# Performance work log

Hardware: AMD Instinct MI355X
Metric: run time of the kernel (lower is better)

The kernel has to match this reference:

```python
import jax, jax.numpy as jnp
import numpy as np

B, N, CTX = 1024, 50000, 96
D_IN, D_MAIN, D_BLOCK, OUT = 128, 256, 512, 10
EPS = 1e-5


def _ln(h, g, b):
    m = jnp.mean(h, -1, keepdims=True)
    v = jnp.var(h, -1, keepdims=True)
    return (h - m) / jnp.sqrt(v + EPS) * g + b


def _forward(fl, candidate_y, context_size):
    (x, candidate_x, W_lin, b_lin,
     enc0_W1, enc0_b1, enc0_W2, enc0_b2,
     enc1_g, enc1_b, enc1_W1, enc1_b1, enc1_W2, enc1_b2,
     mix_g, mix_b, K_W, K_b, label_emb,
     T_W1, T_b1, T_W2,
     p0_g, p0_b, p0_W1, p0_b1, p0_W2, p0_b2,
     p1_g, p1_b, p1_W1, p1_b1, p1_W2, p1_b2,
     head_g, head_b, head_W, head_bias) = fl

    def block(h, g, b, W1, b1, W2, b2, prenorm):
        t = _ln(h, g, b) if prenorm else h
        return h + (jax.nn.relu(t @ W1 + b1) @ W2 + b2)

    def encode(h):
        h = h @ W_lin + b_lin
        h = block(h, None, None, enc0_W1, enc0_b1, enc0_W2, enc0_b2, False)
        h = block(h, enc1_g, enc1_b, enc1_W1, enc1_b1, enc1_W2, enc1_b2, True)
        k = _ln(h, mix_g, mix_b) @ K_W + K_b
        return h, k

    cand_k = encode(candidate_x)[1]          # [N, D]
    h, k = encode(x)                          # [B, D] each
    # exact L2 kNN search (faiss IndexFlatL2 equivalent), indices are non-differentiable
    d2 = (jnp.sum(k * k, -1, keepdims=True) - 2.0 * (k @ cand_k.T)
          + jnp.sum(cand_k * cand_k, -1))    # [B, N]
    idx = jax.lax.stop_gradient(jax.lax.top_k(-d2, context_size)[1])  # [B, C]
    ck = cand_k[idx]                          # [B, C, D]
    sim = (-jnp.sum(k * k, -1, keepdims=True)
           + 2.0 * jnp.einsum('bd,bcd->bc', k, ck)
           - jnp.sum(ck * ck, -1))            # [B, C]
    probs = jax.nn.softmax(sim, -1)
    y_emb = label_emb[candidate_y[idx]]       # [B, C, D]
    vals = y_emb + jax.nn.relu((k[:, None, :] - ck) @ T_W1 + T_b1) @ T_W2
    h = h + jnp.einsum('bc,bcd->bd', probs, vals)
    h = block(h, p0_g, p0_b, p0_W1, p0_b1, p0_W2, p0_b2, True)
    h = block(h, p1_g, p1_b, p1_W1, p1_b1, p1_W2, p1_b2, True)
    return jax.nn.relu(_ln(h, head_g, head_b)) @ head_W + head_bias


def setup_inputs() -> dict:
    key = jax.random.key(0)
    ks = iter(jax.random.split(key, 64))
    def W(shape, fan_in):
        s = 1.0 / np.sqrt(fan_in)
        return jax.random.uniform(next(ks), shape, jnp.float32, -s, s)
    z = lambda *s: jnp.zeros(s, jnp.float32)
    o = lambda *s: jnp.ones(s, jnp.float32)
    d = {
        'x': jax.random.normal(next(ks), (B, D_IN), jnp.float32),
        'candidate_x': jax.random.normal(next(ks), (N, D_IN), jnp.float32),
        'candidate_y': jax.random.randint(next(ks), (N,), 0, OUT),
        'context_size': CTX,
        'W_lin': W((D_IN, D_MAIN), D_IN), 'b_lin': z(D_MAIN),
        'enc0_W1': W((D_MAIN, D_BLOCK), D_MAIN), 'enc0_b1': z(D_BLOCK),
        'enc0_W2': W((D_BLOCK, D_MAIN), D_BLOCK), 'enc0_b2': z(D_MAIN),
        'enc1_g': o(D_MAIN), 'enc1_b': z(D_MAIN),
        'enc1_W1': W((D_MAIN, D_BLOCK), D_MAIN), 'enc1_b1': z(D_BLOCK),
        'enc1_W2': W((D_BLOCK, D_MAIN), D_BLOCK), 'enc1_b2': z(D_MAIN),
        'mix_g': o(D_MAIN), 'mix_b': z(D_MAIN),
        'K_W': W((D_MAIN, D_MAIN), D_MAIN), 'K_b': z(D_MAIN),
        'label_emb': jax.random.uniform(next(ks), (OUT, D_MAIN), jnp.float32, -1.0, 1.0),
        'T_W1': W((D_MAIN, D_BLOCK), D_MAIN), 'T_b1': z(D_BLOCK),
        'T_W2': W((D_BLOCK, D_MAIN), D_BLOCK),
        'p0_g': o(D_MAIN), 'p0_b': z(D_MAIN),
        'p0_W1': W((D_MAIN, D_BLOCK), D_MAIN), 'p0_b1': z(D_BLOCK),
        'p0_W2': W((D_BLOCK, D_MAIN), D_BLOCK), 'p0_b2': z(D_MAIN),
        'p1_g': o(D_MAIN), 'p1_b': z(D_MAIN),
        'p1_W1': W((D_MAIN, D_BLOCK), D_MAIN), 'p1_b1': z(D_BLOCK),
        'p1_W2': W((D_BLOCK, D_MAIN), D_BLOCK), 'p1_b2': z(D_MAIN),
        'head_g': o(D_MAIN), 'head_b': z(D_MAIN),
        'head_W': W((D_MAIN, OUT), D_MAIN), 'head_bias': z(OUT),
    }
    return d


def reference(x, candidate_x, candidate_y, context_size, W_lin, b_lin,
              enc0_W1, enc0_b1, enc0_W2, enc0_b2,
              enc1_g, enc1_b, enc1_W1, enc1_b1, enc1_W2, enc1_b2,
              mix_g, mix_b, K_W, K_b, label_emb,
              T_W1, T_b1, T_W2,
              p0_g, p0_b, p0_W1, p0_b1, p0_W2, p0_b2,
              p1_g, p1_b, p1_W1, p1_b1, p1_W2, p1_b2,
              head_g, head_b, head_W, head_bias):
    fl = (x, candidate_x, W_lin, b_lin,
          enc0_W1, enc0_b1, enc0_W2, enc0_b2,
          enc1_g, enc1_b, enc1_W1, enc1_b1, enc1_W2, enc1_b2,
          mix_g, mix_b, K_W, K_b, label_emb,
          T_W1, T_b1, T_W2,
          p0_g, p0_b, p0_W1, p0_b1, p0_W2, p0_b2,
          p1_g, p1_b, p1_W1, p1_b1, p1_W2, p1_b2,
          head_g, head_b, head_W, head_bias)
    return _forward(fl, candidate_y, context_size)
```

## Files before the change

### kernel.cpp

```cpp
#include <hip/hip_runtime.h>
#include <hip/hip_bf16.h>
#include <cstdint>
#include <cstddef>

#define B_ROWS 1024
#define N_CAND 50000
#define CTX    96
#define D_IN   128
#define D_MAIN 256
#define D_BLOCK 512
#define N_OUT  10
#define LN_EPS 1e-5f
#define MAXTIE 4096
#define NTOT   (N_CAND + B_ROWS)

typedef unsigned short u16;
typedef __attribute__((ext_vector_type(8))) short bf16x8;
typedef __attribute__((ext_vector_type(4))) float f32x4;

__device__ __forceinline__ u16 bf16_bits(float f) {
    __hip_bfloat16 h = __float2bfloat16(f);
    return *reinterpret_cast<u16*>(&h);
}
__device__ __forceinline__ float bits_to_f32(u16 b) {
    unsigned u = ((unsigned)b) << 16;
    return __uint_as_float(u);
}
__device__ __forceinline__ void split_f32(float v, u16& h, u16& l) {
    h = bf16_bits(v);
    l = bf16_bits(v - bits_to_f32(h));
}
__device__ __forceinline__ float join_f32(u16 h, u16 l) {
    return bits_to_f32(h) + bits_to_f32(l);
}
__device__ __forceinline__ unsigned f2u_mono(float f) {
    unsigned u = __float_as_uint(f);
    return u ^ ((u & 0x80000000u) ? 0xFFFFFFFFu : 0x80000000u);
}

__device__ __forceinline__ void load_lds_16B(const void* gp, void* lp) {
    __builtin_amdgcn_global_load_lds((const __attribute__((address_space(1))) void*)gp,
                                     (__attribute__((address_space(3))) void*)lp,
                                     16, 0, 0);
}

template<bool RELU, bool HAS_BIAS, bool HAS_RES, bool KEY16,
         bool OUT_F32, bool OUT_SPLIT, bool OUT_B16, bool A_LO, bool B_LO, bool MXFAST>
__global__ __launch_bounds__(512)
void gemm_split_nt(const u16* __restrict__ Ah, const u16* __restrict__ Al,
                   const u16* __restrict__ Bh, const u16* __restrict__ Bl,
                   const float* __restrict__ bias, const float* __restrict__ Rm,
                   float* __restrict__ Cf, u16* __restrict__ Ch, u16* __restrict__ Cl,
                   int M, int N, int K)
{
    constexpr int N_LOAD = (2 + (A_LO ? 1 : 0) + (B_LO ? 1 : 0)) * 4096;
    constexpr bool STAGED = KEY16 || OUT_SPLIT || OUT_B16;
    constexpr int CS_STRIDE = 136;
    constexpr int CS_SIZE = 128 * CS_STRIDE;
    constexpr int SM_MIN = STAGED ? CS_SIZE : 0;
    constexpr int SM_U16 = (2 * N_LOAD > SM_MIN) ? 2 * N_LOAD : SM_MIN;
    __shared__ __align__(16) u16 smem[SM_U16];

    constexpr int offAsl = A_LO ? 4096 : 0;
    constexpr int offBsh = 4096 * (1 + (A_LO ? 1 : 0));
    constexpr int offBsl = offBsh + (B_LO ? 4096 : 0);

    const int tid  = threadIdx.x;
    const int wave = tid >> 6, lane = tid & 63;

    int bm, bn;
    if constexpr (MXFAST) {
        const unsigned nbm = gridDim.x;
        const unsigned total = nbm * gridDim.y;
        const unsigned h = blockIdx.x + nbm * blockIdx.y;
        unsigned mi = blockIdx.x, ni = blockIdx.y;
        if ((total & 7u) == 0u) {
            const unsigned per = total >> 3;
            const unsigned virt = (h & 7u) * per + (h >> 3);
            mi = virt % nbm;
            ni = virt / nbm;
        }
        bm = (int)mi * 128; bn = (int)ni * 128;
    } else {
        bm = blockIdx.y * 128; bn = blockIdx.x * 128;
    }

    const int wm = (wave >> 2) * 64, wn = (wave & 3) * 32;
    const int l16 = lane & 15, quad = lane >> 4;

    const int srow = lane >> 2;
    const int scol = (lane & 3) * 8;

    const int r0 = wave * 16 + srow;
    int ga0 = bm + r0; if (ga0 > M - 1) ga0 = M - 1;
    int gb0 = bn + r0; if (gb0 > N - 1) gb0 = N - 1;
    const size_t offA0 = (size_t)ga0 * K + scol;
    const size_t offB0 = (size_t)gb0 * K + scol;
    const int ldsR0 = (wave * 16) * 32;

    auto stage = [&](int buf, int k0) {
        u16* base = smem + buf * N_LOAD;
        load_lds_16B(Ah + offA0 + k0, &base[ldsR0]);
        if constexpr (A_LO)
            load_lds_16B(Al + offA0 + k0, &base[offAsl + ldsR0]);
        load_lds_16B(Bh + offB0 + k0, &base[offBsh + ldsR0]);
        if constexpr (B_LO)
            load_lds_16B(Bl + offB0 + k0, &base[offBsl + ldsR0]);
    };

    f32x4 acc[4][2];
    #pragma unroll
    for (int i = 0; i < 4; ++i)
        #pragma unroll
        for (int j = 0; j < 2; ++j)
            acc[i][j] = (f32x4){0.f, 0.f, 0.f, 0.f};

    stage(0, 0);
    int cur = 0;
    for (int k0 = 0; k0 < K; k0 += 32) {
        __syncthreads();

        const u16* Ash = smem + cur * N_LOAD;
        const u16* Asl = Ash + offAsl;
        const u16* Bsh = Ash + offBsh;
        const u16* Bsl = Ash + offBsl;

        bf16x8 ah[4], al[4], bh[2], bl[2];
        #pragma unroll
        for (int i = 0; i < 4; ++i) {
            ah[i] = *(const bf16x8*)&Ash[(wm + i * 16 + l16) * 32 + quad * 8];
            if constexpr (A_LO)
                al[i] = *(const bf16x8*)&Asl[(wm + i * 16 + l16) * 32 + quad * 8];
        }
        #pragma unroll
        for (int j = 0; j < 2; ++j) {
            bh[j] = *(const bf16x8*)&Bsh[(wn + j * 16 + l16) * 32 + quad * 8];
            if constexpr (B_LO)
                bl[j] = *(const bf16x8*)&Bsl[(wn + j * 16 + l16) * 32 + quad * 8];
        }

        if (k0 + 32 < K) stage(cur ^ 1, k0 + 32);

        #pragma unroll
        for (int i = 0; i < 4; ++i)
            #pragma unroll
            for (int j = 0; j < 2; ++j) {
                acc[i][j] = __builtin_amdgcn_mfma_f32_16x16x32_bf16(ah[i], bh[j], acc[i][j], 0, 0, 0);
                if constexpr (A_LO)
                    acc[i][j] = __builtin_amdgcn_mfma_f32_16x16x32_bf16(al[i], bh[j], acc[i][j], 0, 0, 0);
                if constexpr (B_LO)
                    acc[i][j] = __builtin_amdgcn_mfma_f32_16x16x32_bf16(ah[i], bl[j], acc[i][j], 0, 0, 0);
            }
        cur ^= 1;
    }

    float bvj[2];
    #pragma unroll
    for (int j = 0; j < 2; ++j) {
        const int n = bn + wn + j * 16 + l16;
        bvj[j] = ((HAS_BIAS || KEY16) && n < N) ? bias[n] : 0.f;
    }
    auto compute = [&](int i, int j, int r) -> float {
        float v = acc[i][j][r];
        if (KEY16) return -2.f * v + bvj[j];
        if (HAS_BIAS) v += bvj[j];
        if (RELU)     v = fmaxf(v, 0.f);
        if (HAS_RES) {
            const int n = bn + wn + j * 16 + l16;
            const int m = bm + wm + i * 16 + quad * 4 + r;
            v += Rm[(size_t)m * N + n];
        }
        return v;
    };

    if constexpr (OUT_F32) {
        #pragma unroll
        for (int j = 0; j < 2; ++j) {
            const int n = bn + wn + j * 16 + l16;
            if (n >= N) continue;
            #pragma unroll
            for (int i = 0; i < 4; ++i)
                #pragma unroll
                for (int r = 0; r < 4; ++r) {
                    const int m = bm + wm + i * 16 + quad * 4 + r;
                    if (m >= M) continue;
                    Cf[(size_t)m * N + n] = compute(i, j, r);
                }
        }
    }

    if constexpr (STAGED) {
        u16* Cs = smem;
        const int phases = OUT_SPLIT ? 2 : 1;
        for (int ph = 0; ph < phases; ++ph) {
            __syncthreads();
            #pragma unroll
            for (int j = 0; j < 2; ++j) {
                const int nl = wn + j * 16 + l16;
                if (bn + nl >= N) continue;
                #pragma unroll
                for (int i = 0; i < 4; ++i)
                    #pragma unroll
                    for (int r = 0; r < 4; ++r) {
                        const int ml = wm + i * 16 + quad * 4 + r;
                        if (bm + ml >= M) continue;
                        const float v = compute(i, j, r);
                        u16 out;
                        if (KEY16)        out = (u16)(f2u_mono(v) >> 16);
                        else if (OUT_B16) out = bf16_bits(v);
                        else { u16 h, l; split_f32(v, h, l); out = ph ? l : h; }
                        Cs[ml * CS_STRIDE + nl] = out;
                    }
            }
            __syncthreads();
            u16* dstB = (OUT_SPLIT && ph) ? Cl : Ch;
            const int row = tid >> 2, seg = (tid & 3) * 32;
            const int m = bm + row;
            if (m < M) {
                const int ncols = N - bn;
                u16* dst = dstB + (size_t)m * N + bn + seg;
                const u16* srcp = &Cs[row * CS_STRIDE + seg];
                if (ncols >= 128) {
                    #pragma unroll
                    for (int c = 0; c < 4; ++c)
                        *reinterpret_cast<uint4*>(dst + c * 8) =
                            *reinterpret_cast<const uint4*>(srcp + c * 8);
                } else {
                    for (int e = 0; e < 32; ++e)
                        if (seg + e < ncols) dst[e] = srcp[e];
                }
            }
        }
    }
}

__global__ __launch_bounds__(256)
void gemm_head(const float* __restrict__ A, const float* __restrict__ Bm,
               const float* __restrict__ bias, float* __restrict__ C,
               int M, int N, int K)
{
    __shared__ float As[16][64];
    __shared__ float Bs[16][64];
    const int tid = threadIdx.x;
    const int bm = blockIdx.y * 64;

    const int a_m = tid >> 2;
    const int a_k = (tid & 3) << 2;
    const int b_k = tid >> 4;
    const int b_n = (tid & 15) << 2;
    const int my = (tid >> 4) << 2;
    const int nx = (tid & 15) << 2;

    float acc[4][4] = {};

    for (int k0 = 0; k0 < K; k0 += 16) {
        float4 av = make_float4(0.f,0.f,0.f,0.f);
        const int gm = bm + a_m;
        if (gm < M) av = *(const float4*)(A + (size_t)gm * K + k0 + a_k);
        As[a_k+0][a_m]=av.x; As[a_k+1][a_m]=av.y; As[a_k+2][a_m]=av.z; As[a_k+3][a_m]=av.w;

        float4 bv = make_float4(0.f,0.f,0.f,0.f);
        const float* bp = Bm + (size_t)(k0 + b_k) * N + b_n;
        if (b_n + 0 < N) bv.x = bp[0];
        if (b_n + 1 < N) bv.y = bp[1];
        if (b_n + 2 < N) bv.z = bp[2];
        if (b_n + 3 < N) bv.w = bp[3];
        *(float4*)&Bs[b_k][b_n] = bv;

        __syncthreads();
        #pragma unroll
        for (int k = 0; k < 16; ++k) {
            const float4 a4 = *(const float4*)&As[k][my];
            const float4 b4 = *(const float4*)&Bs[k][nx];
            const float a[4] = {a4.x,a4.y,a4.z,a4.w};
            const float b[4] = {b4.x,b4.y,b4.z,b4.w};
            #pragma unroll
            for (int i = 0; i < 4; ++i)
                #pragma unroll
                for (int j = 0; j < 4; ++j)
                    acc[i][j] = fmaf(a[i], b[j], acc[i][j]);
        }
        __syncthreads();
    }

    #pragma unroll
    for (int i = 0; i < 4; ++i) {
        const int m = bm + my + i;
        if (m >= M) continue;
        #pragma unroll
        for (int j = 0; j < 4; ++j) {
            const int n = nx + j;
            if (n >= N) continue;
            C[(size_t)m * N + n] = acc[i][j] + bias[n];
        }
    }
}

template<bool RELU, bool OUT_SPLIT>
__global__ __launch_bounds__(256)
void ln_kernel(const float* __restrict__ X, const float* __restrict__ g,
               const float* __restrict__ b, float* __restrict__ Yf,
               u16* __restrict__ Yh, u16* __restrict__ Yl)
{
    const int row = blockIdx.x, tid = threadIdx.x;
    const float x = X[(size_t)row * D_MAIN + tid];
    __shared__ float red[4];
    const int lane = tid & 63, wid = tid >> 6;

    float s = x;
    #pragma unroll
    for (int off = 32; off; off >>= 1) s += __shfl_down(s, off, 64);
    if (lane == 0) red[wid] = s;
    __syncthreads();
    const float mean = (red[0] + red[1] + red[2] + red[3]) * (1.f / D_MAIN);
    __syncthreads();

    const float xm = x - mean;
    s = xm * xm;
    #pragma unroll
    for (int off = 32; off; off >>= 1) s += __shfl_down(s, off, 64);
    if (lane == 0) red[wid] = s;
    __syncthreads();
    const float var = (red[0] + red[1] + red[2] + red[3]) * (1.f / D_MAIN);

    float y = xm / sqrtf(var + LN_EPS) * g[tid] + b[tid];
    if (RELU) y = fmaxf(y, 0.f);
    if (OUT_SPLIT) {
        u16 h, l; split_f32(y, h, l);
        Yh[(size_t)row * D_MAIN + tid] = h;
        Yl[(size_t)row * D_MAIN + tid] = l;
    } else {
        Yf[(size_t)row * D_MAIN + tid] = y;
    }
}

__global__ __launch_bounds__(64)
void cn2_kernel(const u16* __restrict__ ckh, const u16* __restrict__ ckl,
                float* __restrict__ out)
{
    const int row = blockIdx.x, lane = threadIdx.x;
    const ushort4 h4 = *(const ushort4*)(ckh + (size_t)row * D_MAIN + lane * 4);
    const ushort4 l4 = *(const ushort4*)(ckl + (size_t)row * D_MAIN + lane * 4);
    const float c0 = join_f32(h4.x, l4.x), c1 = join_f32(h4.y, l4.y);
    const float c2 = join_f32(h4.z, l4.z), c3 = join_f32(h4.w, l4.w);
    float s = c0*c0 + c1*c1 + c2*c2 + c3*c3;
    #pragma unroll
    for (int off = 32; off; off >>= 1) s += __shfl_down(s, off, 64);
    if (lane == 0) out[row] = s;
}

__global__ __launch_bounds__(256)
void f32_to_split_kernel(const float* __restrict__ src, u16* __restrict__ hi,
                         u16* __restrict__ lo, int n)
{
    int i = blockIdx.x * 256 + threadIdx.x;
    if (i < n) {
        u16 h, l; split_f32(src[i], h, l);
        hi[i] = h; lo[i] = l;
    }
}

struct TrD { const float* s; u16* dh; u16* dl; int R; int C; };
struct TrDs { TrD d[11]; };

__global__ __launch_bounds__(256)
void transpose_all_kernel(TrDs descs)
{
    const TrD D = descs.d[blockIdx.y];
    const int n = D.R * D.C;
    int idx = blockIdx.x * 256 + threadIdx.x;
    if (idx < n) {
        const int r = idx / D.C, c = idx % D.C;
        u16 h, l; split_f32(D.s[idx], h, l);
        D.dh[(size_t)c * D.R + r] = h;
        D.dl[(size_t)c * D.R + r] = l;
    }
}

__global__ __launch_bounds__(256)
void copy_rows_kernel(const float* __restrict__ src, float* __restrict__ dst, int n)
{
    int i = blockIdx.x * 256 + threadIdx.x;
    if (i < n) dst[i] = src[i];
}

__global__ __launch_bounds__(1024)
void topk96_u16_kernel(const u16* __restrict__ keys, int* __restrict__ idx_out,
                       int* __restrict__ tiebuf, int* __restrict__ tiecnt,
                       int* __restrict__ lesscnt)
{
    const int row = blockIdx.x;
    const u16* krow = keys + (size_t)row * N_CAND;
    const int tid = threadIdx.x;
    const int rep = tid & 63;

    __shared__ unsigned hist[256 * 64];
    __shared__ unsigned hsum[256];
    __shared__ unsigned sh_bin, sh_need;
    __shared__ int cntLess, cntEq;

    #pragma unroll
    for (int i = 0; i < 16; ++i) hist[tid + i * 1024] = 0;
    __syncthreads();
    for (int i = tid; i < N_CAND / 8; i += 1024) {
        const uint4 v = ((const uint4*)krow)[i];
        const unsigned w[4] = {v.x, v.y, v.z, v.w};
        #pragma unroll
        for (int e = 0; e < 4; ++e) {
            atomicAdd(&hist[(((w[e] >> 8) & 0xFFu)) * 64 + rep], 1u);
            atomicAdd(&hist[((w[e] >> 24)) * 64 + rep], 1u);
        }
    }
    __syncthreads();
    if (tid < 256) {
        unsigned s = 0;
        #pragma unroll
        for (int r = 0; r < 64; ++r) s += hist[tid * 64 + ((r + tid) & 63)];
        hsum[tid] = s;
    }
    __syncthreads();
    int need = CTX;
    if (tid < 64) {
        const unsigned b0 = hsum[tid*4+0], b1 = hsum[tid*4+1],
                       b2 = hsum[tid*4+2], b3 = hsum[tid*4+3];
        const unsigned lsum = b0 + b1 + b2 + b3;
        unsigned pre = lsum;
        #pragma unroll
        for (int off = 1; off < 64; off <<= 1) {
            const unsigned t = __shfl_up(pre, off, 64);
            if (tid >= off) pre += t;
        }
        const unsigned excl = pre - lsum;
        const unsigned nd = (unsigned)need;
        if (excl < nd && excl + lsum >= nd) {
            unsigned bin, rem;
            if      (excl + b0 >= nd)           { bin = tid*4+0; rem = nd - excl; }
            else if (excl + b0 + b1 >= nd)      { bin = tid*4+1; rem = nd - excl - b0; }
            else if (excl + b0 + b1 + b2 >= nd) { bin = tid*4+2; rem = nd - excl - b0 - b1; }
            else                                { bin = tid*4+3; rem = nd - excl - b0 - b1 - b2; }
            sh_bin = bin; sh_need = rem;
        }
    }
    __syncthreads();
    const unsigned hb = sh_bin;
    need = (int)sh_need;
    __syncthreads();

    #pragma unroll
    for (int i = 0; i < 16; ++i) hist[tid + i * 1024] = 0;
    __syncthreads();
    for (int i = tid; i < N_CAND / 8; i += 1024) {
        const uint4 v = ((const uint4*)krow)[i];
        const unsigned w[4] = {v.x, v.y, v.z, v.w};
        #pragma unroll
        for (int e = 0; e < 4; ++e) {
            const unsigned k0 = w[e] & 0xFFFFu, k1 = w[e] >> 16;
            if ((k0 >> 8) == hb) atomicAdd(&hist[(k0 & 255u) * 64 + rep], 1u);
            if ((k1 >> 8) == hb) atomicAdd(&hist[(k1 & 255u) * 64 + rep], 1u);
        }
    }
    __syncthreads();
    if (tid < 256) {
        unsigned s = 0;
        #pragma unroll
        for (int r = 0; r < 64; ++r) s += hist[tid * 64 + ((r + tid) & 63)];
        hsum[tid] = s;
    }
    __syncthreads();
    if (tid < 64) {
        const unsigned b0 = hsum[tid*4+0], b1 = hsum[tid*4+1],
                       b2 = hsum[tid*4+2], b3 = hsum[tid*4+3];
        const unsigned lsum = b0 + b1 + b2 + b3;
        unsigned pre = lsum;
        #pragma unroll
        for (int off = 1; off < 64; off <<= 1) {
            const unsigned t = __shfl_up(pre, off, 64);
            if (tid >= off) pre += t;
        }
        const unsigned excl = pre - lsum;
        const unsigned nd = (unsigned)need;
        if (excl < nd && excl + lsum >= nd) {
            unsigned bin, rem;
            if      (excl + b0 >= nd)           { bin = tid*4+0; rem = nd - excl; }
            else if (excl + b0 + b1 >= nd)      { bin = tid*4+1; rem = nd - excl - b0; }
            else if (excl + b0 + b1 + b2 >= nd) { bin = tid*4+2; rem = nd - excl - b0 - b1; }
            else                                { bin = tid*4+3; rem = nd - excl - b0 - b1 - b2; }
            sh_bin = bin; sh_need = rem;
        }
    }
    __syncthreads();
    const unsigned T16 = (hb << 8) | sh_bin;
    need = (int)sh_need;

    if (tid == 0) { cntLess = 0; cntEq = 0; }
    __syncthreads();

    for (int i = tid; i < N_CAND / 8; i += 1024) {
        const uint4 v = ((const uint4*)krow)[i];
        const unsigned w[4] = {v.x, v.y, v.z, v.w};
        #pragma unroll
        for (int e = 0; e < 4; ++e) {
            const unsigned k0 = w[e] & 0xFFFFu, k1 = w[e] >> 16;
            const int n0 = i * 8 + e * 2, n1 = n0 + 1;
            if (k0 < T16) {
                const int p = atomicAdd(&cntLess, 1);
                idx_out[row * CTX + p] = n0;
            } else if (k0 == T16) {
                const int p = atomicAdd(&cntEq, 1);
                if (p < MAXTIE) tiebuf[(size_t)row * MAXTIE + p] = n0;
            }
            if (k1 < T16) {
                const int p = atomicAdd(&cntLess, 1);
                idx_out[row * CTX + p] = n1;
            } else if (k1 == T16) {
                const int p = atomicAdd(&cntEq, 1);
                if (p < MAXTIE) tiebuf[(size_t)row * MAXTIE + p] = n1;
            }
        }
    }
    __syncthreads();
    if (tid == 0) {
        lesscnt[row] = cntLess;
        tiecnt[row] = (cntEq < MAXTIE) ? cntEq : MAXTIE;
    }
}

__global__ __launch_bounds__(256)
void select_kernel(const u16* __restrict__ kh, const u16* __restrict__ kl,
                   const u16* __restrict__ ckh, const u16* __restrict__ ckl,
                   const float* __restrict__ ck2,
                   const int* __restrict__ tiebuf, const int* __restrict__ tiecnt,
                   const int* __restrict__ lesscnt,
                   int* __restrict__ idx_out, float* __restrict__ probs)
{
    const int row = blockIdx.x;
    const int tid = threadIdx.x;
    const int T = tiecnt[row];
    const int less = lesscnt[row];
    const int need = CTX - less;

    __shared__ float kvs[D_MAIN];
    __shared__ int   sel[CTX];
    __shared__ float svals[CTX];
    __shared__ float sv[MAXTIE];
    __shared__ unsigned hist[256];
    __shared__ unsigned sh_bin, sh_need;
    __shared__ int c1, c2;

    if (tid < D_MAIN)
        kvs[tid] = join_f32(kh[(size_t)row * D_MAIN + tid], kl[(size_t)row * D_MAIN + tid]);
    if (tid < CTX && tid < less) sel[tid] = idx_out[row * CTX + tid];
    __syncthreads();

    if (T <= need) {
        for (int t = tid; t < T; t += 256) {
            sel[less + t] = tiebuf[(size_t)row * MAXTIE + t];
            idx_out[row * CTX + less + t] = sel[less + t];
        }
    } else {
        for (int t = tid; t < T; t += 256) {
            const int c = tiebuf[(size_t)row * MAXTIE + t];
            const u16* ch = ckh + (size_t)c * D_MAIN;
            const u16* cl = ckl + (size_t)c * D_MAIN;
            float s = 0.f;
            #pragma unroll 8
            for (int d = 0; d < D_MAIN; d += 4) {
                const ushort4 h4 = *(const ushort4*)(ch + d);
                const ushort4 l4 = *(const ushort4*)(cl + d);
                s += kvs[d+0] * join_f32(h4.x, l4.x) + kvs[d+1] * join_f32(h4.y, l4.y)
                   + kvs[d+2] * join_f32(h4.z, l4.z) + kvs[d+3] * join_f32(h4.w, l4.w);
            }
            sv[t] = ck2[c] - 2.f * s;
        }
        __syncthreads();

        unsigned prefix = 0;
        int plen = 0;
        int nd = need;
        for (int pass = 0; pass < 4; ++pass) {
            const int shift = 24 - 8 * pass;
            hist[tid] = 0;
            __syncthreads();
            for (int t = tid; t < T; t += 256) {
                const unsigned u = f2u_mono(sv[t]);
                if (plen == 0 || (u >> (32 - plen)) == prefix)
                    atomicAdd(&hist[(u >> shift) & 255u], 1u);
            }
            __syncthreads();
            if (tid < 64) {
                const unsigned b0 = hist[tid*4+0], b1 = hist[tid*4+1],
                               b2 = hist[tid*4+2], b3 = hist[tid*4+3];
                const unsigned lsum = b0 + b1 + b2 + b3;
                unsigned pre = lsum;
                #pragma unroll
                for (int off = 1; off < 64; off <<= 1) {
                    const unsigned tt = __shfl_up(pre, off, 64);
                    if (tid >= off) pre += tt;
                }
                const unsigned excl = pre - lsum;
                const unsigned ndu = (unsigned)nd;
                if (excl < ndu && excl + lsum >= ndu) {
                    unsigned bin, rem;
                    if      (excl + b0 >= ndu)           { bin = tid*4+0; rem = ndu - excl; }
                    else if (excl + b0 + b1 >= ndu)      { bin = tid*4+1; rem = ndu - excl - b0; }
                    else if (excl + b0 + b1 + b2 >= ndu) { bin = tid*4+2; rem = ndu - excl - b0 - b1; }
                    else                                 { bin = tid*4+3; rem = ndu - excl - b0 - b1 - b2; }
                    sh_bin = bin; sh_need = rem;
                }
            }
            __syncthreads();
            prefix = (prefix << 8) | sh_bin;
            nd = (int)sh_need;
            plen += 8;
            __syncthreads();
        }
        const unsigned Tf = prefix;
        const int nl2 = need - nd;
        if (tid == 0) { c1 = 0; c2 = 0; }
        __syncthreads();
        for (int t = tid; t < T; t += 256) {
            const unsigned u = f2u_mono(sv[t]);
            if (u < Tf) {
                const int p = atomicAdd(&c1, 1);
                sel[less + p] = tiebuf[(size_t)row * MAXTIE + t];
                idx_out[row * CTX + less + p] = sel[less + p];
            } else if (u == Tf) {
                const int p = atomicAdd(&c2, 1);
                if (p < nd) {
                    sel[less + nl2 + p] = tiebuf[(size_t)row * MAXTIE + t];
                    idx_out[row * CTX + less + nl2 + p] = sel[less + nl2 + p];
                }
            }
        }
    }
    __syncthreads();

    const int wv = tid >> 6, lane = tid & 63;
    #pragma unroll
    for (int k = 0; k < 24; k += 4) {
        int ids[4];
        ushort4 h4[4], l4[4];
        #pragma unroll
        for (int u = 0; u < 4; ++u) {
            const int c = wv + 4 * (k + u);
            ids[u] = sel[c];
            h4[u] = *(const ushort4*)(ckh + (size_t)ids[u] * D_MAIN + lane * 4);
            l4[u] = *(const ushort4*)(ckl + (size_t)ids[u] * D_MAIN + lane * 4);
        }
        #pragma unroll
        for (int u = 0; u < 4; ++u) {
            const int c = wv + 4 * (k + u);
            float s = kvs[lane*4+0] * join_f32(h4[u].x, l4[u].x)
                    + kvs[lane*4+1] * join_f32(h4[u].y, l4[u].y)
                    + kvs[lane*4+2] * join_f32(h4[u].z, l4[u].z)
                    + kvs[lane*4+3] * join_f32(h4[u].w, l4[u].w);
            #pragma unroll
            for (int off = 32; off; off >>= 1) s += __shfl_down(s, off, 64);
            if (lane == 0) svals[c] = ck2[ids[u]] - 2.f * s;
        }
    }
    __syncthreads();

    if (tid < 64) {
        const float a = -svals[tid];
        const float b = (tid < 32) ? -svals[64 + tid] : -1e30f;
        float m = fmaxf(a, b);
        #pragma unroll
        for (int off = 32; off; off >>= 1) m = fmaxf(m, __shfl_xor(m, off, 64));
        const float ea = __expf(a - m);
        const float eb = (tid < 32) ? __expf(b - m) : 0.f;
        float ssum = ea + eb;
        #pragma unroll
        for (int off = 32; off; off >>= 1) ssum += __shfl_xor(ssum, off, 64);
        const float inv = 1.f / ssum;
        probs[row * CTX + tid] = ea * inv;
        if (tid < 32) probs[row * CTX + 64 + tid] = eb * inv;
    }
}

__global__ __launch_bounds__(256)
void tmix_kernel(const float* __restrict__ Q, const float* __restrict__ b1,
                 const float* __restrict__ W2, const float* __restrict__ probs,
                 const int* __restrict__ idx, const int* __restrict__ cy,
                 const float* __restrict__ label_emb, float* __restrict__ h)
{
    const int b = blockIdx.x, tid = threadIdx.x;
    __shared__ float pr[CTX];
    __shared__ int   ids[CTX];
    __shared__ int   labs[CTX];
    __shared__ float lemb[N_OUT * D_MAIN];
    __shared__ float uv[D_BLOCK];
    if (tid < CTX) {
        const int id = idx[b * CTX + tid];
        ids[tid]  = id;
        pr[tid]   = probs[b * CTX + tid];
        labs[tid] = cy[id];
    }
    for (int i = tid; i < N_OUT * D_MAIN; i += 256) lemb[i] = label_emb[i];
    __syncthreads();

    const int j0 = tid * 2;
    const float2 pb = *(const float2*)(Q + (size_t)(N_CAND + b) * D_BLOCK + j0);
    const float p0 = pb.x + b1[j0];
    const float p1 = pb.y + b1[j0 + 1];
    float a0 = 0.f, a1 = 0.f, ahd = 0.f;
    #pragma unroll 4
    for (int c = 0; c < CTX; ++c) {
        const float p = pr[c];
        const float2 q = *(const float2*)(Q + (size_t)ids[c] * D_BLOCK + j0);
        a0  = fmaf(p, fmaxf(p0 - q.x, 0.f), a0);
        a1  = fmaf(p, fmaxf(p1 - q.y, 0.f), a1);
        ahd = fmaf(p, lemb[labs[c] * D_MAIN + tid], ahd);
    }
    uv[j0] = a0;
    uv[j0 + 1] = a1;
    __syncthreads();

    float o = ahd;
    #pragma unroll 8
    for (int k = 0; k < D_BLOCK; ++k)
        o = fmaf(uv[k], W2[(size_t)k * D_MAIN + tid], o);
    h[(size_t)b * D_MAIN + tid] += o;
}

static inline dim3 g128(int M, int N) {
    return dim3((unsigned)((N + 127) / 128), (unsigned)((M + 127) / 128));
}

struct EncW {
    const u16 *WlinTh, *WlinTl, *e0W1Th, *e0W1Tl, *e0W2Th, *e0W2Tl,
              *e1W1Th, *e1W1Tl, *e1W2Th, *e1W2Tl, *KWTh, *KWTl;
    const float *b_lin, *e0b1, *e0b2, *e1g, *e1b, *e1b1, *e1b2, *mixg, *mixb, *Kb;
};

static void encode_rows_split(const u16* Xh, const u16* Xl, int R, const EncW& w,
                              float* H, u16* Hh, u16* Hl, u16* Th, u16* Tl,
                              u16* TNh, u16* TNl, u16* Kh, u16* Kl,
                              hipStream_t stream)
{
    dim3 blk(512);
    gemm_split_nt<false,true,false,false, true,true,false, true,true,false><<<g128(R, D_MAIN), blk, 0, stream>>>(
        Xh, Xl, w.WlinTh, w.WlinTl, w.b_lin, nullptr, H, Hh, Hl, R, D_MAIN, D_IN);
    gemm_split_nt<true,true,false,false, false,true,false, true,true,false><<<g128(R, D_BLOCK), blk, 0, stream>>>(
        Hh, Hl, w.e0W1Th, w.e0W1Tl, w.e0b1, nullptr, nullptr, Th, Tl, R, D_BLOCK, D_MAIN);
    gemm_split_nt<false,true,true,false, true,false,false, true,true,false><<<g128(R, D_MAIN), blk, 0, stream>>>(
        Th, Tl, w.e0W2Th, w.e0W2Tl, w.e0b2, H, H, nullptr, nullptr, R, D_MAIN, D_BLOCK);
    ln_kernel<false,true><<<R, 256, 0, stream>>>(H, w.e1g, w.e1b, nullptr, TNh, TNl);
    gemm_split_nt<true,true,false,false, false,true,false, true,true,false><<<g128(R, D_BLOCK), blk, 0, stream>>>(
        TNh, TNl, w.e1W1Th, w.e1W1Tl, w.e1b1, nullptr, nullptr, Th, Tl, R, D_BLOCK, D_MAIN);
    gemm_split_nt<false,true,true,false, true,false,false, true,true,false><<<g128(R, D_MAIN), blk, 0, stream>>>(
        Th, Tl, w.e1W2Th, w.e1W2Tl, w.e1b2, H, H, nullptr, nullptr, R, D_MAIN, D_BLOCK);
    ln_kernel<false,true><<<R, 256, 0, stream>>>(H, w.mixg, w.mixb, nullptr, TNh, TNl);
    gemm_split_nt<false,true,false,false, false,true,false, true,true,false><<<g128(R, D_MAIN), blk, 0, stream>>>(
        TNh, TNl, w.KWTh, w.KWTl, w.Kb, nullptr, nullptr, Kh, Kl, R, D_MAIN, D_MAIN);
}

extern "C" void kernel_launch(void* const* d_in, const int* in_sizes, int n_in,
                              void* d_out, int out_size, void* d_ws, size_t ws_size,
                              hipStream_t stream)
{
    const float* x        = (const float*)d_in[0];
    const float* cand_x   = (const float*)d_in[1];
    const int*   cand_y   = (const int*)  d_in[2];
    const float* W_lin    = (const float*)d_in[4];
    const float* b_lin    = (const float*)d_in[5];
    const float* e0W1     = (const float*)d_in[6];
    const float* e0b1     = (const float*)d_in[7];
    const float* e0W2     = (const float*)d_in[8];
    const float* e0b2     = (const float*)d_in[9];
    const float* e1g      = (const float*)d_in[10];
    const float* e1b      = (const float*)d_in[11];
    const float* e1W1     = (const float*)d_in[12];
    const float* e1b1     = (const float*)d_in[13];
    const float* e1W2     = (const float*)d_in[14];
    const float* e1b2     = (const float*)d_in[15];
    const float* mixg     = (const float*)d_in[16];
    const float* mixb     = (const float*)d_in[17];
    const float* K_W      = (const float*)d_in[18];
    const float* K_b      = (const float*)d_in[19];
    const float* label_emb= (const float*)d_in[20];
    const float* T_W1     = (const float*)d_in[21];
    const float* T_b1     = (const float*)d_in[22];
    const float* T_W2     = (const float*)d_in[23];
    const float* p0g      = (const float*)d_in[24];
    const float* p0b      = (const float*)d_in[25];
    const float* p0W1     = (const float*)d_in[26];
    const float* p0b1     = (const float*)d_in[27];
    const float* p0W2     = (const float*)d_in[28];
    const float* p0b2     = (const float*)d_in[29];
    const float* p1g      = (const float*)d_in[30];
    const float* p1b      = (const float*)d_in[31];
    const float* p1W1     = (const float*)d_in[32];
    const float* p1b1     = (const float*)d_in[33];
    const float* p1W2     = (const float*)d_in[34];
    const float* p1b2     = (const float*)d_in[35];
    const float* headg    = (const float*)d_in[36];
    const float* headb    = (const float*)d_in[37];
    const float* head_W   = (const float*)d_in[38];
    const float* head_bias= (const float*)d_in[39];

    char* ws = (char*)d_ws;
    size_t off = 0;
    auto alloc = [&](size_t bytes) -> char* {
        char* p = ws + off;
        off += (bytes + 255) & ~(size_t)255;
        return p;
    };

    u16* in_h   = (u16*)alloc((size_t)NTOT * D_IN * 2);
    u16* in_l   = (u16*)alloc((size_t)NTOT * D_IN * 2);
    u16* allk_h = (u16*)alloc((size_t)NTOT * D_MAIN * 2);
    u16* allk_l = (u16*)alloc((size_t)NTOT * D_MAIN * 2);
    float* ck2  = (float*)alloc((size_t)N_CAND * 4);
    float* h_x  = (float*)alloc((size_t)B_ROWS * D_MAIN * 4);
    float* tn_x = (float*)alloc((size_t)B_ROWS * D_MAIN * 4);
    u16* tnb_h  = (u16*)alloc((size_t)B_ROWS * D_MAIN * 2);
    u16* tnb_l  = (u16*)alloc((size_t)B_ROWS * D_MAIN * 2);
    u16* tb_h   = (u16*)alloc((size_t)B_ROWS * D_BLOCK * 2);
    u16* tb_l   = (u16*)alloc((size_t)B_ROWS * D_BLOCK * 2);
    int*   idx  = (int*)  alloc((size_t)B_ROWS * CTX * 4);
    float* probs= (float*)alloc((size_t)B_ROWS * CTX * 4);
    int* tiecnt = (int*)  alloc((size_t)B_ROWS * 4);
    int* lesscnt= (int*)  alloc((size_t)B_ROWS * 4);

    auto allocW = [&](int R, int C, u16** h, u16** l) {
        *h = (u16*)alloc((size_t)R * C * 2);
        *l = (u16*)alloc((size_t)R * C * 2);
    };
    u16 *WlinTh, *WlinTl, *e0W1Th, *e0W1Tl, *e0W2Th, *e0W2Tl,
        *e1W1Th, *e1W1Tl, *e1W2Th, *e1W2Tl, *KWTh, *KWTl,
        *TW1Th, *TW1Tl,
        *p0W1Th, *p0W1Tl, *p0W2Th, *p0W2Tl, *p1W1Th, *p1W1Tl, *p1W2Th, *p1W2Tl;
    allocW(D_IN,   D_MAIN, &WlinTh, &WlinTl);
    allocW(D_MAIN, D_BLOCK,&e0W1Th, &e0W1Tl);
    allocW(D_BLOCK,D_MAIN, &e0W2Th, &e0W2Tl);
    allocW(D_MAIN, D_BLOCK,&e1W1Th, &e1W1Tl);
    allocW(D_BLOCK,D_MAIN, &e1W2Th, &e1W2Tl);
    allocW(D_MAIN, D_MAIN, &KWTh,   &KWTl);
    allocW(D_MAIN, D_BLOCK,&TW1Th,  &TW1Tl);
    allocW(D_MAIN, D_BLOCK,&p0W1Th, &p0W1Tl);
    allocW(D_BLOCK,D_MAIN, &p0W2Th, &p0W2Tl);
    allocW(D_MAIN, D_BLOCK,&p1W1Th, &p1W1Tl);
    allocW(D_BLOCK,D_MAIN, &p1W2Th, &p1W2Tl);

    int* tiebuf = (int*)alloc((size_t)B_ROWS * MAXTIE * 4);

    u16* k_x_h = allk_h + (size_t)N_CAND * D_MAIN;
    u16* k_x_l = allk_l + (size_t)N_CAND * D_MAIN;
    u16* x_in_h = in_h + (size_t)N_CAND * D_IN;
    u16* x_in_l = in_l + (size_t)N_CAND * D_IN;

    const size_t pool_avail = (ws_size > off) ? (ws_size - off) : 0;
    int rc_enc = (int)(pool_avail / 5120);
    if (rc_enc > NTOT) rc_enc = NTOT;
    if (rc_enc < 6250) rc_enc = 6250;
    int mb_ch = (int)(pool_avail / ((size_t)2 * N_CAND));
    if (mb_ch > B_ROWS) mb_ch = B_ROWS;
    mb_ch &= ~127;
    if (mb_ch < 128)    mb_ch = 128;

    char* pool = ws + off;
    dim3 blk(256);
    dim3 blkg(512);

    {
        f32_to_split_kernel<<<(N_CAND*D_IN + 255)/256, blk, 0, stream>>>(cand_x, in_h, in_l, N_CAND*D_IN);
        f32_to_split_kernel<<<(B_ROWS*D_IN + 255)/256, blk, 0, stream>>>(x, x_in_h, x_in_l, B_ROWS*D_IN);
        TrDs tr;
        tr.d[0]  = { W_lin, WlinTh, WlinTl, D_IN,   D_MAIN };
        tr.d[1]  = { e0W1,  e0W1Th, e0W1Tl, D_MAIN, D_BLOCK };
        tr.d[2]  = { e0W2,  e0W2Th, e0W2Tl, D_BLOCK,D_MAIN };
        tr.d[3]  = { e1W1,  e1W1Th, e1W1Tl, D_MAIN, D_BLOCK };
        tr.d[4]  = { e1W2,  e1W2Th, e1W2Tl, D_BLOCK,D_MAIN };
        tr.d[5]  = { K_W,   KWTh,   KWTl,   D_MAIN, D_MAIN };
        tr.d[6]  = { T_W1,  TW1Th,  TW1Tl,  D_MAIN, D_BLOCK };
        tr.d[7]  = { p0W1,  p0W1Th, p0W1Tl, D_MAIN, D_BLOCK };
        tr.d[8]  = { p0W2,  p0W2Th, p0W2Tl, D_BLOCK,D_MAIN };
        tr.d[9]  = { p1W1,  p1W1Th, p1W1Tl, D_MAIN, D_BLOCK };
        tr.d[10] = { p1W2,  p1W2Th, p1W2Tl, D_BLOCK,D_MAIN };
        transpose_all_kernel<<<dim3(512, 11), blk, 0, stream>>>(tr);
    }

    EncW w = { WlinTh, WlinTl, e0W1Th, e0W1Tl, e0W2Th, e0W2Tl,
               e1W1Th, e1W1Tl, e1W2Th, e1W2Tl, KWTh, KWTl,
               b_lin, e0b1, e0b2, e1g, e1b, e1b1, e1b2, mixg, mixb, K_b };

    for (int r0 = 0; r0 < NTOT; r0 += rc_enc) {
        const int R = (NTOT - r0 < rc_enc) ? (NTOT - r0) : rc_enc;
        char* p = pool;
        float* Hc = (float*)p;        p += (size_t)rc_enc * D_MAIN * 4;
        u16* Hh  = (u16*)p;           p += (size_t)rc_enc * D_MAIN * 2;
        u16* Hl  = (u16*)p;           p += (size_t)rc_enc * D_MAIN * 2;
        u16* Th  = (u16*)p;           p += (size_t)rc_enc * D_BLOCK * 2;
        u16* Tl  = (u16*)p;           p += (size_t)rc_enc * D_BLOCK * 2;
        u16* TNh = (u16*)p;           p += (size_t)rc_enc * D_MAIN * 2;
        u16* TNl = (u16*)p;
        encode_rows_split(in_h + (size_t)r0 * D_IN, in_l + (size_t)r0 * D_IN,
                          R, w, Hc, Hh, Hl, Th, Tl, TNh, TNl,
                          allk_h + (size_t)r0 * D_MAIN,
                          allk_l + (size_t)r0 * D_MAIN, stream);
        const int lo = (r0 > N_CAND) ? r0 : N_CAND;
        const int hi = (r0 + R < NTOT) ? r0 + R : NTOT;
        if (lo < hi) {
            const int n = (hi - lo) * D_MAIN;
            copy_rows_kernel<<<(n + 255)/256, blk, 0, stream>>>(
                Hc + (size_t)(lo - r0) * D_MAIN, h_x + (size_t)(lo - N_CAND) * D_MAIN, n);
        }
    }

    cn2_kernel<<<N_CAND, 64, 0, stream>>>(allk_h, allk_l, ck2);

    for (int m0 = 0; m0 < B_ROWS; m0 += mb_ch) {
        const int R = (B_ROWS - m0 < mb_ch) ? (B_ROWS - m0) : mb_ch;
        u16* s_keys = (u16*)pool;
        dim3 grid((unsigned)((R + 127) / 128), (unsigned)((N_CAND + 127) / 128));
        gemm_split_nt<false,false,false,true, false,false,false, false,false,true><<<grid, blkg, 0, stream>>>(
            k_x_h + (size_t)m0 * D_MAIN, nullptr,
            allk_h, nullptr, ck2, nullptr, nullptr, s_keys, nullptr,
            R, N_CAND, D_MAIN);
        topk96_u16_kernel<<<R, 1024, 0, stream>>>(
            s_keys, idx + m0 * CTX, tiebuf + (size_t)m0 * MAXTIE,
            tiecnt + m0, lesscnt + m0);
    }

    select_kernel<<<B_ROWS, 256, 0, stream>>>(k_x_h, k_x_l, allk_h, allk_l, ck2,
                                              tiebuf, tiecnt, lesscnt, idx, probs);

    float* Qbuf = (float*)tiebuf;
    gemm_split_nt<false,false,false,false, true,false,false, true,true,false><<<g128(NTOT, D_BLOCK), blkg, 0, stream>>>(
        allk_h, allk_l, TW1Th, TW1Tl, nullptr, nullptr, Qbuf, nullptr, nullptr,
        NTOT, D_BLOCK, D_MAIN);
    tmix_kernel<<<B_ROWS, 256, 0, stream>>>(Qbuf, T_b1, T_W2, probs, idx,
                                            cand_y, label_emb, h_x);

    ln_kernel<false,true><<<B_ROWS, 256, 0, stream>>>(h_x, p0g, p0b, nullptr, tnb_h, tnb_l);
    gemm_split_nt<true,true,false,false, false,true,false, true,true,false><<<g128(B_ROWS, D_BLOCK), blkg, 0, stream>>>(
        tnb_h, tnb_l, p0W1Th, p0W1Tl, p0b1, nullptr, nullptr, tb_h, tb_l, B_ROWS, D_BLOCK, D_MAIN);
    gemm_split_nt<false,true,true,false, true,false,false, true,true,false><<<g128(B_ROWS, D_MAIN), blkg, 0, stream>>>(
        tb_h, tb_l, p0W2Th, p0W2Tl, p0b2, h_x, h_x, nullptr, nullptr, B_ROWS, D_MAIN, D_BLOCK);
    ln_kernel<false,true><<<B_ROWS, 256, 0, stream>>>(h_x, p1g, p1b, nullptr, tnb_h, tnb_l);
    gemm_split_nt<true,true,false,false, false,true,false, true,true,false><<<g128(B_ROWS, D_BLOCK), blkg, 0, stream>>>(
        tnb_h, tnb_l, p1W1Th, p1W1Tl, p1b1, nullptr, nullptr, tb_h, tb_l, B_ROWS, D_BLOCK, D_MAIN);
    gemm_split_nt<false,true,true,false, true,false,false, true,true,false><<<g128(B_ROWS, D_MAIN), blkg, 0, stream>>>(
        tb_h, tb_l, p1W2Th, p1W2Tl, p1b2, h_x, h_x, nullptr, nullptr, B_ROWS, D_MAIN, D_BLOCK);

    ln_kernel<true,false><<<B_ROWS, 256, 0, stream>>>(h_x, headg, headb, tn_x, nullptr, nullptr);
    gemm_head<<<dim3(1, (B_ROWS + 63) / 64), blk, 0, stream>>>(
        tn_x, head_W, head_bias, (float*)d_out, B_ROWS, N_OUT, D_MAIN);
}
```

Before: 1.093 ms.

## Use 1024-thread blocks in split GEMM with 32x32 per-wave tiles

```diff
diff --git a/kernel.cpp b/kernel.cpp
--- a/kernel.cpp
+++ b/kernel.cpp
@@ -46,14 +46,17 @@
 
 template<bool RELU, bool HAS_BIAS, bool HAS_RES, bool KEY16,
          bool OUT_F32, bool OUT_SPLIT, bool OUT_B16, bool A_LO, bool B_LO, bool MXFAST>
-__global__ __launch_bounds__(512)
+__global__ __launch_bounds__(1024)
 void gemm_split_nt(const u16* __restrict__ Ah, const u16* __restrict__ Al,
                    const u16* __restrict__ Bh, const u16* __restrict__ Bl,
                    const float* __restrict__ bias, const float* __restrict__ Rm,
                    float* __restrict__ Cf, u16* __restrict__ Ch, u16* __restrict__ Cl,
                    int M, int N, int K)
 {
-    constexpr int N_LOAD = (2 + (A_LO ? 1 : 0) + (B_LO ? 1 : 0)) * 4096;
+    constexpr int nArrA = 1 + (A_LO ? 1 : 0);
+    constexpr int nArrB = 1 + (B_LO ? 1 : 0);
+    constexpr int NARR  = nArrA + nArrB;
+    constexpr int N_LOAD = NARR * 4096;
     constexpr bool STAGED = KEY16 || OUT_SPLIT || OUT_B16;
     constexpr int CS_STRIDE = 136;
     constexpr int CS_SIZE = 128 * CS_STRIDE;
@@ -62,7 +65,7 @@
     __shared__ __align__(16) u16 smem[SM_U16];
 
     constexpr int offAsl = A_LO ? 4096 : 0;
-    constexpr int offBsh = 4096 * (1 + (A_LO ? 1 : 0));
+    constexpr int offBsh = 4096 * nArrA;
     constexpr int offBsl = offBsh + (B_LO ? 4096 : 0);
 
     const int tid  = threadIdx.x;
@@ -85,32 +88,48 @@
         bm = blockIdx.y * 128; bn = blockIdx.x * 128;
     }
 
-    const int wm = (wave >> 2) * 64, wn = (wave & 3) * 32;
+    const int wm = (wave >> 2) * 32, wn = (wave & 3) * 32;
     const int l16 = lane & 15, quad = lane >> 4;
 
     const int srow = lane >> 2;
     const int scol = (lane & 3) * 8;
 
-    const int r0 = wave * 16 + srow;
-    int ga0 = bm + r0; if (ga0 > M - 1) ga0 = M - 1;
-    int gb0 = bn + r0; if (gb0 > N - 1) gb0 = N - 1;
-    const size_t offA0 = (size_t)ga0 * K + scol;
-    const size_t offB0 = (size_t)gb0 * K + scol;
-    const int ldsR0 = (wave * 16) * 32;
+    auto segAddr = [&](int s, const u16*& gp, int& lo) {
+        const int a = s >> 3, rb = s & 7;
+        const bool isA = (a < nArrA);
+        int row = (isA ? bm : bn) + rb * 16 + srow;
+        const int mx = (isA ? M : N) - 1;
+        if (row > mx) row = mx;
+        const u16* base;
+        if (a == 0)            base = Ah;
+        else if (a == 1)       base = (nArrA > 1) ? Al : Bh;
+        else if (a == 2)       base = (nArrA > 1) ? Bh : Bl;
+        else                   base = Bl;
+        gp = base + (size_t)row * K + scol;
+        lo = a * 4096 + rb * 512;
+    };
+
+    const u16* sg0; int sl0;
+    segAddr(wave, sg0, sl0);
+    const u16* sg1 = nullptr; int sl1 = 0;
+    constexpr bool SEG1_ALL  = (NARR == 4);
+    constexpr bool SEG1_HALF = (NARR == 3);
+    if constexpr (SEG1_ALL)  segAddr(wave + 16, sg1, sl1);
+    if constexpr (SEG1_HALF) { if (wave < 8) segAddr(wave + 16, sg1, sl1); }
 
     auto stage = [&](int buf, int k0) {
         u16* base = smem + buf * N_LOAD;
-        load_lds_16B(Ah + offA0 + k0, &base[ldsR0]);
-        if constexpr (A_LO)
-            load_lds_16B(Al + offA0 + k0, &base[offAsl + ldsR0]);
-        load_lds_16B(Bh + offB0 + k0, &base[offBsh + ldsR0]);
-        if constexpr (B_LO)
-            load_lds_16B(Bl + offB0 + k0, &base[offBsl + ldsR0]);
+        load_lds_16B(sg0 + k0, &base[sl0]);
+        if constexpr (SEG1_ALL)
+            load_lds_16B(sg1 + k0, &base[sl1]);
+        if constexpr (SEG1_HALF) {
+            if (wave < 8) load_lds_16B(sg1 + k0, &base[sl1]);
+        }
     };
 
-    f32x4 acc[4][2];
+    f32x4 acc[2][2];
     #pragma unroll
-    for (int i = 0; i < 4; ++i)
+    for (int i = 0; i < 2; ++i)
         #pragma unroll
         for (int j = 0; j < 2; ++j)
             acc[i][j] = (f32x4){0.f, 0.f, 0.f, 0.f};
@@ -125,9 +144,9 @@
         const u16* Bsh = Ash + offBsh;
         const u16* Bsl = Ash + offBsl;
 
-        bf16x8 ah[4], al[4], bh[2], bl[2];
-        #pragma unroll
-        for (int i = 0; i < 4; ++i) {
+        bf16x8 ah[2], al[2], bh[2], bl[2];
+        #pragma unroll
+        for (int i = 0; i < 2; ++i) {
             ah[i] = *(const bf16x8*)&Ash[(wm + i * 16 + l16) * 32 + quad * 8];
             if constexpr (A_LO)
                 al[i] = *(const bf16x8*)&Asl[(wm + i * 16 + l16) * 32 + quad * 8];
@@ -142,7 +161,7 @@
         if (k0 + 32 < K) stage(cur ^ 1, k0 + 32);
 
         #pragma unroll
-        for (int i = 0; i < 4; ++i)
+        for (int i = 0; i < 2; ++i)
             #pragma unroll
             for (int j = 0; j < 2; ++j) {
                 acc[i][j] = __builtin_amdgcn_mfma_f32_16x16x32_bf16(ah[i], bh[j], acc[i][j], 0, 0, 0);
@@ -179,7 +198,7 @@
             const int n = bn + wn + j * 16 + l16;
             if (n >= N) continue;
             #pragma unroll
-            for (int i = 0; i < 4; ++i)
+            for (int i = 0; i < 2; ++i)
                 #pragma unroll
                 for (int r = 0; r < 4; ++r) {
                     const int m = bm + wm + i * 16 + quad * 4 + r;
@@ -199,7 +218,7 @@
                 const int nl = wn + j * 16 + l16;
                 if (bn + nl >= N) continue;
                 #pragma unroll
-                for (int i = 0; i < 4; ++i)
+                for (int i = 0; i < 2; ++i)
                     #pragma unroll
                     for (int r = 0; r < 4; ++r) {
                         const int ml = wm + i * 16 + quad * 4 + r;
@@ -214,7 +233,7 @@
             }
             __syncthreads();
             u16* dstB = (OUT_SPLIT && ph) ? Cl : Ch;
-            const int row = tid >> 2, seg = (tid & 3) * 32;
+            const int row = tid >> 3, seg = (tid & 7) * 16;
             const int m = bm + row;
             if (m < M) {
                 const int ncols = N - bn;
@@ -222,11 +241,11 @@
                 const u16* srcp = &Cs[row * CS_STRIDE + seg];
                 if (ncols >= 128) {
                     #pragma unroll
-                    for (int c = 0; c < 4; ++c)
+                    for (int c = 0; c < 2; ++c)
                         *reinterpret_cast<uint4*>(dst + c * 8) =
                             *reinterpret_cast<const uint4*>(srcp + c * 8);
                 } else {
-                    for (int e = 0; e < 32; ++e)
+                    for (int e = 0; e < 16; ++e)
                         if (seg + e < ncols) dst[e] = srcp[e];
                 }
             }
@@ -738,7 +757,7 @@
                               u16* TNh, u16* TNl, u16* Kh, u16* Kl,
                               hipStream_t stream)
 {
-    dim3 blk(512);
+    dim3 blk(1024);
     gemm_split_nt<false,true,false,false, true,true,false, true,true,false><<<g128(R, D_MAIN), blk, 0, stream>>>(
         Xh, Xl, w.WlinTh, w.WlinTl, w.b_lin, nullptr, H, Hh, Hl, R, D_MAIN, D_IN);
     gemm_split_nt<true,true,false,false, false,true,false, true,true,false><<<g128(R, D_BLOCK), blk, 0, stream>>>(
@@ -861,7 +880,7 @@
 
     char* pool = ws + off;
     dim3 blk(256);
-    dim3 blkg(512);
+    dim3 blkg(1024);
 
     {
         f32_to_split_kernel<<<(N_CAND*D_IN + 255)/256, blk, 0, stream>>>(cand_x, in_h, in_l, N_CAND*D_IN);
```

Result: faster. 1.014 ms (-7.2%).
